# Kernel tuning notes

Hardware: AMD Instinct MI355X
Metric: run time of the kernel (lower is better)

The kernel has to match this reference:

```python
import jax, jax.numpy as jnp
from jax import lax
import numpy as np

EMBED = 20
FILTERS = 16
KSIZES = (1, 3, 5, 7, 9)
LIN_IN = 7 * len(KSIZES) * FILTERS  # 560
LIN_DIM = 64
SEQ_LENS = {'pep': 12, 'a1': 7, 'a2': 8, 'a3': 16, 'b1': 6, 'b2': 7, 'b3': 18}
BATCH = 16384


def setup_inputs() -> dict:
    key = jax.random.key(0)
    keys = jax.random.split(key, 16)
    inp = {}
    for i, (name, L) in enumerate(SEQ_LENS.items()):
        inp[name] = jax.random.normal(keys[i], (BATCH, EMBED, L), dtype=jnp.float32)
    # Conv weights: one stacked array per kernel size, [7 sequences, FILTERS, EMBED, k]
    for j, k in enumerate(KSIZES):
        inp[f'Wk{k}'] = jax.random.normal(keys[7 + j], (7, FILTERS, EMBED, k), dtype=jnp.float32) * 0.1
    inp['lin1_w'] = jax.random.normal(keys[12], (LIN_DIM, LIN_IN), dtype=jnp.float32) * 0.05
    inp['lin1_b'] = jnp.zeros((LIN_DIM,), dtype=jnp.float32)
    inp['lin2_w'] = jax.random.normal(keys[13], (1, LIN_DIM), dtype=jnp.float32) * 0.1
    inp['lin2_b'] = jnp.zeros((1,), dtype=jnp.float32)
    return inp


def _conv_relu_gmax(x, w):
    # x: [B, C, L], w: [F, C, k] -> SAME conv + ReLU + global max over length -> [B, F]
    y = lax.conv_general_dilated(x, w, window_strides=(1,), padding='SAME',
                                 dimension_numbers=('NCH', 'OIH', 'NCH'))
    return jnp.max(jax.nn.relu(y), axis=-1)


def _branch(x, ws):
    # x scaled by 1/5 as in the torch forward; concat pooled features over kernel sizes
    x = x / 5.0
    return jnp.concatenate([_conv_relu_gmax(x, w) for w in ws], axis=1)  # [B, 5*F]


def reference(pep, a1, a2, a3, b1, b2, b3, Wk1, Wk3, Wk5, Wk7, Wk9,
              lin1_w, lin1_b, lin2_w, lin2_b):
    seqs = [pep, a1, a2, a3, b1, b2, b3]
    Wks = [Wk1, Wk3, Wk5, Wk7, Wk9]
    feats = jnp.concatenate(
        [_branch(seqs[i], [W[i] for W in Wks]) for i in range(7)], axis=1)  # [B, 560]
    # Dropout is identity at inference.
    h = jax.nn.sigmoid(feats @ lin1_w.T + lin1_b)  # [B, 64]
    out = h @ lin2_w.T + lin2_b                    # [B, 1]
    return out.reshape(-1)                          # [B]
```

## Files before the change

### kernel.cpp

```cpp
#include <hip/hip_runtime.h>
#include <stdint.h>
#include <stddef.h>

typedef short bfrag __attribute__((ext_vector_type(8)));
typedef float f32x4 __attribute__((ext_vector_type(4)));

#define FSTRIDE 576
#define NSEQ 7

__constant__ int c_L[NSEQ]     = {12, 7, 8, 16, 6, 7, 18};
__constant__ int c_shift[NSEQ] = {4, 3, 3, 4, 3, 3, 5};
__constant__ int c_bpt[NSEQ]   = {1, 2, 2, 1, 2, 2, 1};
__constant__ int c_ks[5]       = {1, 3, 5, 7, 9};

#define SLO0 3
#define SLO1 2
#define SLO2 1
#define SLO3 0
#define SLO4 0
#define SN0 1
#define SN1 3
#define SN2 5
#define SN3 6
#define SN4 7

static __device__ __forceinline__ unsigned short f2bf(float f) {
  unsigned int u = __float_as_uint(f);
  u += 0x7FFFu + ((u >> 16) & 1u);
  return (unsigned short)(u >> 16);
}

struct PrepArgs {
  const float* Wk[5];
  const float* lin1_w;
  bfrag* Wpack;
  bfrag* lin1pack;
};

__global__ __launch_bounds__(256) void prep_kernel(PrepArgs a) {
  int tid = blockIdx.x * 256 + threadIdx.x;
  const int NW = NSEQ * 5 * 7 * 64;
  if (tid < NW) {
    int lane = tid & 63, rest = tid >> 6;
    int step = rest % 7, nt = (rest / 7) % 5, seq = rest / 35;
    int quad = lane >> 4, f = lane & 15;
    int ks = c_ks[nt], off = (9 - ks) >> 1;
    const float* W = a.Wk[nt];
    bfrag s;
#pragma unroll
    for (int j = 0; j < 8; ++j) {
      int k = step * 32 + quad * 8 + j;
      int t = k / 24, c = k % 24;
      int tap = t - off;
      float val = 0.f;
      if (c < 20 && tap >= 0 && tap < ks)
        val = W[((seq * 16 + f) * 20 + c) * ks + tap] * 0.2f;
      s[j] = (short)f2bf(val);
    }
    a.Wpack[tid] = s;
  } else if (tid < NW + 4 * 18 * 64) {
    int t2 = tid - NW;
    int lane = t2 & 63, rest = t2 >> 6;
    int step = rest % 18, nt = rest / 18;
    int quad = lane >> 4, col = lane & 15;
    int n = nt * 16 + col;
    bfrag s;
#pragma unroll
    for (int j = 0; j < 8; ++j) {
      int k = step * 32 + quad * 8 + j;
      float val = (k < 560) ? a.lin1_w[n * 560 + k] : 0.f;
      s[j] = (short)f2bf(val);
    }
    a.lin1pack[t2] = s;
  }
}

struct ConvArgs {
  const float* x[NSEQ];
  const bfrag* Wpack;
  unsigned short* feats;
};

template <int TBBv, int Pv, int SEQ0, int MT>
__global__ __launch_bounds__(256, 3) void conv_kernel(ConvArgs a) {
  __shared__ unsigned short xl[TBBv * Pv * 24];
  const int seq = SEQ0 + blockIdx.y;
  const int L = c_L[seq], shift = c_shift[seq], bpt = c_bpt[seq];
  const int njobs = ((TBBv << shift) >> 4) / MT;
  const int b0 = blockIdx.x * TBBv;
  const int tid = threadIdx.x;
  const float* xg = a.x[seq];

  const int nwords = TBBv * Pv * 24 / 2;
  for (int i = tid; i < nwords; i += 256) ((unsigned int*)xl)[i] = 0u;
  __syncthreads();
  for (int r = tid; r < TBBv * 20; r += 256) {
    int b = r / 20, c = r % 20;
    const float* src = xg + (size_t)((b0 + b) * 20 + c) * L;
    unsigned short* dst = xl + (b * Pv + 4) * 24 + c;
    for (int xi = 0; xi < L; ++xi) dst[xi * 24] = f2bf(src[xi]);
  }
  if (SEQ0 == 0 && blockIdx.y == 0) {
    for (int i = tid; i < TBBv * 16; i += 256)
      a.feats[(size_t)(b0 + i / 16) * FSTRIDE + 560 + (i % 16)] = 0;
  }
  __syncthreads();

  const int wave = tid >> 6, lane = tid & 63, quad = lane >> 4, m = lane & 15;
  const int lmask = (1 << shift) - 1;

  const bfrag* wp = a.Wpack + (size_t)(seq * 5 * 7) * 64 + lane;
  bfrag Bf[22];
  {
    int bi = 0;
#pragma unroll
    for (int i = 0; i < SN0; ++i) Bf[bi++] = wp[(0 * 7 + SLO0 + i) * 64];
#pragma unroll
    for (int i = 0; i < SN1; ++i) Bf[bi++] = wp[(1 * 7 + SLO1 + i) * 64];
#pragma unroll
    for (int i = 0; i < SN2; ++i) Bf[bi++] = wp[(2 * 7 + SLO2 + i) * 64];
#pragma unroll
    for (int i = 0; i < SN3; ++i) Bf[bi++] = wp[(3 * 7 + SLO3 + i) * 64];
#pragma unroll
    for (int i = 0; i < SN4; ++i) Bf[bi++] = wp[(4 * 7 + SLO4 + i) * 64];
  }

  for (int job = wave; job < njobs; job += 4) {
    float v0 = 0.f, v1 = 0.f, v2 = 0.f, v3 = 0.f, v4 = 0.f;
#pragma unroll
    for (int sub = 0; sub < MT; ++sub) {
      int r = (job * MT + sub) * 16 + m;
      int bl = r >> shift, l = r & lmask;
      const unsigned short* arow = &xl[(bl * Pv + l) * 24 + quad * 8];
      f32x4 acc0 = {0.f, 0.f, 0.f, 0.f}, acc1 = acc0, acc2 = acc0, acc3 = acc0, acc4 = acc0;
#pragma unroll
      for (int s = 0; s < 7; ++s) {
        bfrag Af = *(const bfrag*)(arow + s * 32);
        if (s >= SLO0 && s < SLO0 + SN0)
          acc0 = __builtin_amdgcn_mfma_f32_16x16x32_bf16(Af, Bf[0 + s - SLO0], acc0, 0, 0, 0);
        if (s >= SLO1 && s < SLO1 + SN1)
          acc1 = __builtin_amdgcn_mfma_f32_16x16x32_bf16(Af, Bf[1 + s - SLO1], acc1, 0, 0, 0);
        if (s >= SLO2 && s < SLO2 + SN2)
          acc2 = __builtin_amdgcn_mfma_f32_16x16x32_bf16(Af, Bf[4 + s - SLO2], acc2, 0, 0, 0);
        if (s >= SLO3 && s < SLO3 + SN3)
          acc3 = __builtin_amdgcn_mfma_f32_16x16x32_bf16(Af, Bf[9 + s - SLO3], acc3, 0, 0, 0);
        acc4 = __builtin_amdgcn_mfma_f32_16x16x32_bf16(Af, Bf[15 + s], acc4, 0, 0, 0);
      }
#pragma unroll
      for (int r4 = 0; r4 < 4; ++r4) {
        int lrow = ((sub << 4) + quad * 4 + r4) & lmask;
        bool ok = lrow < L;
        v0 = fmaxf(v0, ok ? acc0[r4] : 0.f);
        v1 = fmaxf(v1, ok ? acc1[r4] : 0.f);
        v2 = fmaxf(v2, ok ? acc2[r4] : 0.f);
        v3 = fmaxf(v3, ok ? acc3[r4] : 0.f);
        v4 = fmaxf(v4, ok ? acc4[r4] : 0.f);
      }
    }
    v0 = fmaxf(v0, __shfl_xor(v0, 16));
    v1 = fmaxf(v1, __shfl_xor(v1, 16));
    v2 = fmaxf(v2, __shfl_xor(v2, 16));
    v3 = fmaxf(v3, __shfl_xor(v3, 16));
    v4 = fmaxf(v4, __shfl_xor(v4, 16));
    if (bpt == 1) {
      v0 = fmaxf(v0, __shfl_xor(v0, 32));
      v1 = fmaxf(v1, __shfl_xor(v1, 32));
      v2 = fmaxf(v2, __shfl_xor(v2, 32));
      v3 = fmaxf(v3, __shfl_xor(v3, 32));
      v4 = fmaxf(v4, __shfl_xor(v4, 32));
      if (lane < 16) {
        unsigned short* p = a.feats + (size_t)(b0 + job) * FSTRIDE + seq * 80 + lane;
        p[0] = f2bf(v0); p[16] = f2bf(v1); p[32] = f2bf(v2); p[48] = f2bf(v3); p[64] = f2bf(v4);
      }
    } else {
      if ((lane & 16) == 0) {
        int b = b0 + job * 2 + (lane >> 5);
        unsigned short* p = a.feats + (size_t)b * FSTRIDE + seq * 80 + (lane & 15);
        p[0] = f2bf(v0); p[16] = f2bf(v1); p[32] = f2bf(v2); p[48] = f2bf(v3); p[64] = f2bf(v4);
      }
    }
  }
}

struct MlpArgs {
  const unsigned short* feats;
  const bfrag* lin1pack;
  const float* lin1_b;
  const float* lin2_w;
  const float* lin2_b;
  float* out;
};

__global__ __launch_bounds__(256) void mlp_kernel(MlpArgs a) {
  __shared__ float h[16 * 68];
  __shared__ float w2[64];
  const int tid = threadIdx.x;
  const int b0 = blockIdx.x * 16;
  if (tid < 64) w2[tid] = a.lin2_w[tid];
  const int wave = tid >> 6, lane = tid & 63, quad = lane >> 4, m = lane & 15;
  const int nt = wave;
  const unsigned short* frow = a.feats + (size_t)(b0 + m) * FSTRIDE;
  f32x4 acc = {0.f, 0.f, 0.f, 0.f};
#pragma unroll
  for (int s = 0; s < 18; ++s) {
    bfrag af = *(const bfrag*)(frow + s * 32 + quad * 8);
    bfrag bf = a.lin1pack[(nt * 18 + s) * 64 + lane];
    acc = __builtin_amdgcn_mfma_f32_16x16x32_bf16(af, bf, acc, 0, 0, 0);
  }
  int n = nt * 16 + m;
  float bias = a.lin1_b[n];
#pragma unroll
  for (int r = 0; r < 4; ++r) {
    float pre = acc[r] + bias;
    h[(quad * 4 + r) * 68 + n] = 1.f / (1.f + __expf(-pre));
  }
  __syncthreads();
  int bl = tid >> 4, q = tid & 15;
  const float* hr = &h[bl * 68 + q * 4];
  float s = hr[0] * w2[q * 4] + hr[1] * w2[q * 4 + 1] + hr[2] * w2[q * 4 + 2] + hr[3] * w2[q * 4 + 3];
  s += __shfl_xor(s, 1);
  s += __shfl_xor(s, 2);
  s += __shfl_xor(s, 4);
  s += __shfl_xor(s, 8);
  if (q == 0) a.out[b0 + bl] = s + a.lin2_b[0];
}

extern "C" void kernel_launch(void* const* d_in, const int* in_sizes, int n_in,
                              void* d_out, int out_size, void* d_ws, size_t ws_size,
                              hipStream_t stream) {
  (void)in_sizes; (void)n_in; (void)out_size; (void)ws_size;
  char* ws = (char*)d_ws;
  bfrag* Wpack = (bfrag*)(ws + 0);
  bfrag* lin1pack = (bfrag*)(ws + 262144);
  unsigned short* feats = (unsigned short*)(ws + 393216);

  PrepArgs pa;
  for (int j = 0; j < 5; ++j) pa.Wk[j] = (const float*)d_in[7 + j];
  pa.lin1_w = (const float*)d_in[12];
  pa.Wpack = Wpack;
  pa.lin1pack = lin1pack;
  prep_kernel<<<80, 256, 0, stream>>>(pa);

  ConvArgs ca;
  for (int i = 0; i < NSEQ; ++i) ca.x[i] = (const float*)d_in[i];
  ca.Wpack = Wpack;
  ca.feats = feats;
  conv_kernel<32, 25, 0, 1><<<dim3(16384 / 32, 6), 256, 0, stream>>>(ca);
  conv_kernel<16, 41, 6, 2><<<dim3(16384 / 16, 1), 256, 0, stream>>>(ca);

  MlpArgs ma;
  ma.feats = feats;
  ma.lin1pack = lin1pack;
  ma.lin1_b = (const float*)d_in[13];
  ma.lin2_w = (const float*)d_in[14];
  ma.lin2_b = (const float*)d_in[15];
  ma.out = (float*)d_out;
  mlp_kernel<<<16384 / 16, 256, 0, stream>>>(ma);
}
```

Measured before the change: 205.1 us.

## Merge conv launches into one kernel with per-sequence compile-time specializations

```diff
diff --git a/kernel.cpp b/kernel.cpp
--- a/kernel.cpp
+++ b/kernel.cpp
@@ -8,10 +8,7 @@
 #define FSTRIDE 576
 #define NSEQ 7
 
-__constant__ int c_L[NSEQ]     = {12, 7, 8, 16, 6, 7, 18};
-__constant__ int c_shift[NSEQ] = {4, 3, 3, 4, 3, 3, 5};
-__constant__ int c_bpt[NSEQ]   = {1, 2, 2, 1, 2, 2, 1};
-__constant__ int c_ks[5]       = {1, 3, 5, 7, 9};
+__constant__ int c_ks[5] = {1, 3, 5, 7, 9};
 
 #define SLO0 3
 #define SLO1 2
@@ -81,33 +78,29 @@
   unsigned short* feats;
 };
 
-template <int TBBv, int Pv, int SEQ0, int MT>
-__global__ __launch_bounds__(256, 3) void conv_kernel(ConvArgs a) {
-  __shared__ unsigned short xl[TBBv * Pv * 24];
-  const int seq = SEQ0 + blockIdx.y;
-  const int L = c_L[seq], shift = c_shift[seq], bpt = c_bpt[seq];
-  const int njobs = ((TBBv << shift) >> 4) / MT;
-  const int b0 = blockIdx.x * TBBv;
+template <int Lc, int SHIFTc, int MTc>
+__device__ __forceinline__ void conv_body(unsigned short* xl, const ConvArgs& a,
+                                          const int seq, const int b0) {
+  constexpr int TBB = 16, P = 41;
   const int tid = threadIdx.x;
   const float* xg = a.x[seq];
 
-  const int nwords = TBBv * Pv * 24 / 2;
-  for (int i = tid; i < nwords; i += 256) ((unsigned int*)xl)[i] = 0u;
+  for (int i = tid; i < TBB * P * 24 / 2; i += 256) ((unsigned int*)xl)[i] = 0u;
   __syncthreads();
-  for (int r = tid; r < TBBv * 20; r += 256) {
+  for (int r = tid; r < TBB * 20; r += 256) {
     int b = r / 20, c = r % 20;
-    const float* src = xg + (size_t)((b0 + b) * 20 + c) * L;
-    unsigned short* dst = xl + (b * Pv + 4) * 24 + c;
-    for (int xi = 0; xi < L; ++xi) dst[xi * 24] = f2bf(src[xi]);
-  }
-  if (SEQ0 == 0 && blockIdx.y == 0) {
-    for (int i = tid; i < TBBv * 16; i += 256)
+    const float* src = xg + (size_t)((b0 + b) * 20 + c) * Lc;
+    unsigned short* dst = xl + (b * P + 4) * 24 + c;
+#pragma unroll
+    for (int xi = 0; xi < Lc; ++xi) dst[xi * 24] = f2bf(src[xi]);
+  }
+  if (seq == 0) {
+    for (int i = tid; i < TBB * 16; i += 256)
       a.feats[(size_t)(b0 + i / 16) * FSTRIDE + 560 + (i % 16)] = 0;
   }
   __syncthreads();
 
   const int wave = tid >> 6, lane = tid & 63, quad = lane >> 4, m = lane & 15;
-  const int lmask = (1 << shift) - 1;
 
   const bfrag* wp = a.Wpack + (size_t)(seq * 5 * 7) * 64 + lane;
   bfrag Bf[22];
@@ -125,13 +118,18 @@
     for (int i = 0; i < SN4; ++i) Bf[bi++] = wp[(4 * 7 + SLO4 + i) * 64];
   }
 
+  constexpr int njobs = (MTc == 2) ? TBB : ((TBB << SHIFTc) >> 4);
+  constexpr int bpt = (MTc == 1 && SHIFTc == 3) ? 2 : 1;
+  constexpr int lmask = (1 << SHIFTc) - 1;
+
   for (int job = wave; job < njobs; job += 4) {
     float v0 = 0.f, v1 = 0.f, v2 = 0.f, v3 = 0.f, v4 = 0.f;
 #pragma unroll
-    for (int sub = 0; sub < MT; ++sub) {
-      int r = (job * MT + sub) * 16 + m;
-      int bl = r >> shift, l = r & lmask;
-      const unsigned short* arow = &xl[(bl * Pv + l) * 24 + quad * 8];
+    for (int sub = 0; sub < MTc; ++sub) {
+      int bl, l;
+      if (MTc == 2) { bl = job; l = sub * 2 + m; }
+      else { int r = job * 16 + m; bl = r >> SHIFTc; l = r & lmask; }
+      const unsigned short* arow = &xl[(bl * P + l) * 24 + quad * 8];
       f32x4 acc0 = {0.f, 0.f, 0.f, 0.f}, acc1 = acc0, acc2 = acc0, acc3 = acc0, acc4 = acc0;
 #pragma unroll
       for (int s = 0; s < 7; ++s) {
@@ -148,8 +146,7 @@
       }
 #pragma unroll
       for (int r4 = 0; r4 < 4; ++r4) {
-        int lrow = ((sub << 4) + quad * 4 + r4) & lmask;
-        bool ok = lrow < L;
+        bool ok = (MTc == 2) ? true : (((quad * 4 + r4) & lmask) < Lc);
         v0 = fmaxf(v0, ok ? acc0[r4] : 0.f);
         v1 = fmaxf(v1, ok ? acc1[r4] : 0.f);
         v2 = fmaxf(v2, ok ? acc2[r4] : 0.f);
@@ -182,6 +179,20 @@
   }
 }
 
+__global__ __launch_bounds__(256, 5) void conv_kernel(ConvArgs a) {
+  __shared__ unsigned short xl[16 * 41 * 24];
+  const int b0 = blockIdx.x * 16;
+  switch (blockIdx.y) {
+    case 0: conv_body<12, 4, 1>(xl, a, 0, b0); break;
+    case 1: conv_body< 7, 3, 1>(xl, a, 1, b0); break;
+    case 2: conv_body< 8, 3, 1>(xl, a, 2, b0); break;
+    case 3: conv_body<16, 4, 1>(xl, a, 3, b0); break;
+    case 4: conv_body< 6, 3, 1>(xl, a, 4, b0); break;
+    case 5: conv_body< 7, 3, 1>(xl, a, 5, b0); break;
+    default: conv_body<18, 5, 2>(xl, a, 6, b0); break;
+  }
+}
+
 struct MlpArgs {
   const unsigned short* feats;
   const bfrag* lin1pack;
@@ -245,8 +256,7 @@
   for (int i = 0; i < NSEQ; ++i) ca.x[i] = (const float*)d_in[i];
   ca.Wpack = Wpack;
   ca.feats = feats;
-  conv_kernel<32, 25, 0, 1><<<dim3(16384 / 32, 6), 256, 0, stream>>>(ca);
-  conv_kernel<16, 41, 6, 2><<<dim3(16384 / 16, 1), 256, 0, stream>>>(ca);
+  conv_kernel<<<dim3(16384 / 16, NSEQ), 256, 0, stream>>>(ca);
 
   MlpArgs ma;
   ma.feats = feats;
```

Result: slower. 366.7 us (+78.7%).
